# Performance work log

Measured on AMD Instinct MI355X. Metric: run time of the kernel, lower is better.

The kernel has to match this reference:

```python
import jax, jax.numpy as jnp
import numpy as np

EMBED = 1024
HEADS = 16
HDIM = EMBED // HEADS


def setup_inputs() -> dict:
    key = jax.random.key(0)
    ks = jax.random.split(key, 7)
    N, T = 16, 1024
    s = 1.0 / np.sqrt(EMBED)
    X = jax.random.normal(ks[0], (N, T, EMBED), dtype=jnp.float32)
    mask = jax.random.randint(ks[1], (N, 1, T, T), 0, 2, dtype=jnp.int32)
    Wq = jax.random.normal(ks[2], (EMBED, EMBED), dtype=jnp.float32) * s
    Wk = jax.random.normal(ks[3], (EMBED, EMBED), dtype=jnp.float32) * s
    Wv = jax.random.normal(ks[4], (EMBED, EMBED), dtype=jnp.float32) * s
    Wo = jax.random.normal(ks[5], (EMBED, EMBED), dtype=jnp.float32) * s
    bo = jax.random.normal(ks[6], (EMBED,), dtype=jnp.float32) * 0.01
    return {"X": X, "mask": mask, "Wq": Wq, "Wk": Wk, "Wv": Wv, "Wo": Wo, "bo": bo}


def reference(X, mask, Wq, Wk, Wv, Wo, bo):
    N, T, K = X.shape
    # QKV projections (Linear with bias=False): y = x @ W^T
    def proj(W):
        y = jnp.einsum('btk,ok->bto', X, W)          # [N, T, K]
        return y.reshape(N, T, HEADS, HDIM).transpose(0, 2, 1, 3)  # [N, H, T, hd]
    q, k, v = proj(Wq), proj(Wk), proj(Wv)
    # scaled dot-product scores; note source scales by sqrt(embed_size), not sqrt(head_dim)
    scores = jnp.einsum('bhqd,bhkd->bhqk', q, k) / jnp.sqrt(jnp.float32(K))
    scores = jnp.where(mask == 0, jnp.float32(-1e20), scores)
    attn = jax.nn.softmax(scores, axis=-1)
    out = jnp.einsum('bhqk,bhkd->bhqd', attn, v)     # [N, H, T, hd]
    out = out.transpose(0, 2, 1, 3).reshape(N, T, K)  # [N, T, K]
    return jnp.einsum('btk,ok->bto', out, Wo) + bo
```

## Files before the change

kernel.cpp:

```cpp
#include <hip/hip_runtime.h>
#include <hip/hip_bf16.h>

#define EMBED 1024
#define TSEQ  1024
#define NB    16
#define NH    16
#define HD    64
#define MROWS (NB * TSEQ)

typedef __bf16 bf16x8 __attribute__((ext_vector_type(8)));
typedef float  f32x4  __attribute__((ext_vector_type(4)));

__device__ __forceinline__ unsigned int f2bf_bits(float x) {
    union { float f; unsigned int u; } v; v.f = x;
    unsigned int r = v.u + 0x7FFFu + ((v.u >> 16) & 1u);
    return r >> 16;
}

__device__ __forceinline__ int detect_bf16(const unsigned int* __restrict__ X) {
    __shared__ int s_cnt;
    if (threadIdx.x == 0) s_cnt = 0;
    __syncthreads();
    int c = 0;
    const int base = threadIdx.x * 16;
#pragma unroll
    for (int i = 0; i < 16; ++i) {
        unsigned int e = (X[base + i] >> 7) & 0xFFu;
        c += (e >= 100u && e <= 150u) ? 1 : 0;
    }
    atomicAdd(&s_cnt, c);
    __syncthreads();
    return s_cnt >= 2458;
}

__device__ __forceinline__ uint4 load8(const void* __restrict__ p, size_t eoff,
                                       int is_bf16) {
    if (is_bf16) {
        return *(const uint4*)((const __hip_bfloat16*)p + eoff);
    }
    const float* f = (const float*)p + eoff;
    float4 a = *(const float4*)f;
    float4 b = *(const float4*)(f + 4);
    uint4 r;
    r.x = f2bf_bits(a.x) | (f2bf_bits(a.y) << 16);
    r.y = f2bf_bits(a.z) | (f2bf_bits(a.w) << 16);
    r.z = f2bf_bits(b.x) | (f2bf_bits(b.y) << 16);
    r.w = f2bf_bits(b.z) | (f2bf_bits(b.w) << 16);
    return r;
}

__device__ __forceinline__ void gload16(const __hip_bfloat16* g,
                                        __hip_bfloat16* l) {
    __builtin_amdgcn_global_load_lds(
        (const __attribute__((address_space(1))) void*)g,
        (__attribute__((address_space(3))) void*)l, 16, 0, 0);
}

__global__ __launch_bounds__(256) void to_bf16(
    const void* __restrict__ src, __hip_bfloat16* __restrict__ dst,
    int n8, const unsigned int* __restrict__ det)
{
    const int isbf = detect_bf16(det);
    const int i = blockIdx.x * 256 + threadIdx.x;
    if (i < n8) *(uint4*)(dst + (size_t)i * 8) = load8(src, (size_t)i * 8, isbf);
}

#define BK  32
#define LDK 40

template<int AD, int BD>
__global__ __launch_bounds__(256) void gemm_t(
    const void* __restrict__ A,
    const void* __restrict__ W,
    void* __restrict__ C,
    const void* __restrict__ bias,
    const unsigned int* __restrict__ Xdet,
    int a_flex, int out_mode, float cscale)
{
    const int isbf = detect_bf16(Xdet);
    const int a_bf = a_flex ? isbf : 1;

    constexpr int LA = AD ? BK : LDK;
    constexpr int LB = BD ? BK : LDK;
    __shared__ __hip_bfloat16 As[128 * LA];
    __shared__ __hip_bfloat16 Bs[128 * LB];

    const int tid  = threadIdx.x;
    const int lane = tid & 63;
    const int w    = tid >> 6;
    const int wm   = w & 1;
    const int wn   = w >> 1;
    const int m0   = blockIdx.x * 128;
    const int n0   = blockIdx.y * 128;

    const int r0 = tid >> 2;
    const int c0 = (tid & 3) * 8;

    f32x4 acc[4][4];
#pragma unroll
    for (int i = 0; i < 4; ++i)
#pragma unroll
        for (int j = 0; j < 4; ++j)
            acc[i][j] = (f32x4){0.f, 0.f, 0.f, 0.f};

    const int fr = lane & 15;
    const int fq = lane >> 4;

    for (int k0 = 0; k0 < EMBED; k0 += BK) {
        uint4 ra0, ra1, rb0, rb1;
        if constexpr (!AD) {
            ra0 = load8(A, (size_t)(m0 + r0)      * EMBED + c0 + k0, a_bf);
            ra1 = load8(A, (size_t)(m0 + r0 + 64) * EMBED + c0 + k0, a_bf);
        }
        if constexpr (!BD) {
            rb0 = load8(W, (size_t)(n0 + r0)      * EMBED + c0 + k0, isbf);
            rb1 = load8(W, (size_t)(n0 + r0 + 64) * EMBED + c0 + k0, isbf);
        }
        __syncthreads();
        if constexpr (AD) {
            const __hip_bfloat16* Ab =
                (const __hip_bfloat16*)A + (size_t)(m0 + r0) * EMBED + c0 + k0;
            gload16(Ab,                      &As[tid * 8]);
            gload16(Ab + (size_t)64 * EMBED, &As[64 * BK + tid * 8]);
        } else {
            *(uint4*)&As[r0 * LA + c0]        = ra0;
            *(uint4*)&As[(r0 + 64) * LA + c0] = ra1;
        }
        if constexpr (BD) {
            const __hip_bfloat16* Wp =
                (const __hip_bfloat16*)W + (size_t)(n0 + r0) * EMBED + c0 + k0;
            gload16(Wp,                      &Bs[tid * 8]);
            gload16(Wp + (size_t)64 * EMBED, &Bs[64 * BK + tid * 8]);
        } else {
            *(uint4*)&Bs[r0 * LB + c0]        = rb0;
            *(uint4*)&Bs[(r0 + 64) * LB + c0] = rb1;
        }
        __syncthreads();

        bf16x8 af[4], bfr[4];
#pragma unroll
        for (int i = 0; i < 4; ++i) {
            af[i]  = *(const bf16x8*)&As[(wm * 64 + i * 16 + fr) * LA + fq * 8];
            bfr[i] = *(const bf16x8*)&Bs[(wn * 64 + i * 16 + fr) * LB + fq * 8];
        }
#pragma unroll
        for (int i = 0; i < 4; ++i)
#pragma unroll
            for (int j = 0; j < 4; ++j)
                acc[i][j] = __builtin_amdgcn_mfma_f32_16x16x32_bf16(
                    af[i], bfr[j], acc[i][j], 0, 0, 0);
    }

    float bv[4] = {0.f, 0.f, 0.f, 0.f};
    if (bias != nullptr) {
#pragma unroll
        for (int j = 0; j < 4; ++j) {
            const int idx = n0 + wn * 64 + j * 16 + fr;
            bv[j] = isbf ? __bfloat162float(((const __hip_bfloat16*)bias)[idx])
                         : ((const float*)bias)[idx];
        }
    }

    if (out_mode == 2) {
#pragma unroll
        for (int i = 0; i < 4; ++i) {
            const int row = m0 + wm * 64 + i * 16 + fq * 4;
            const int bb = row >> 10, tt = row & 1023;
#pragma unroll
            for (int j = 0; j < 4; ++j) {
                const int col = n0 + wn * 64 + j * 16 + fr;
                const int hh = col >> 6, dd = col & 63;
                uint2 st;
                st.x = f2bf_bits(acc[i][j][0] * cscale) |
                       (f2bf_bits(acc[i][j][1] * cscale) << 16);
                st.y = f2bf_bits(acc[i][j][2] * cscale) |
                       (f2bf_bits(acc[i][j][3] * cscale) << 16);
                *(uint2*)&((__hip_bfloat16*)C)[
                    (((size_t)(bb * NH + hh) * HD + dd) * TSEQ) + tt] = st;
            }
        }
        return;
    }

    const int c_bf = (out_mode == 1) ? isbf : 1;
#pragma unroll
    for (int i = 0; i < 4; ++i) {
        const int row = m0 + wm * 64 + i * 16 + fq * 4;
#pragma unroll
        for (int j = 0; j < 4; ++j) {
            const int col = n0 + wn * 64 + j * 16 + fr;
#pragma unroll
            for (int r = 0; r < 4; ++r) {
                const size_t off = (size_t)(row + r) * EMBED + col;
                const float v = acc[i][j][r] * cscale + bv[j];
                if (c_bf) ((__hip_bfloat16*)C)[off] = __float2bfloat16(v);
                else      ((float*)C)[off] = v;
            }
        }
    }
}

#define QT  64
#define KTL 128
#define KP  72
#define VP  136
#define PP  136

__global__ __launch_bounds__(256) void attn_mfma(
    const __hip_bfloat16* __restrict__ Q,
    const __hip_bfloat16* __restrict__ K,
    const __hip_bfloat16* __restrict__ Vt,
    const int* __restrict__ mask,
    __hip_bfloat16* __restrict__ O)
{
    __shared__ __hip_bfloat16 Ks[KTL * KP];
    __shared__ __hip_bfloat16 Vs[HD * VP];
    __shared__ __hip_bfloat16 Ps[4][16 * PP];

    const int tid  = threadIdx.x;
    const int lane = tid & 63;
    const int w    = tid >> 6;
    const int fr   = lane & 15;
    const int fq   = lane >> 4;
    const int qb = blockIdx.x, h = blockIdx.y, b = blockIdx.z;
    const int q0 = qb * QT;

    const __hip_bfloat16* qptr =
        Q + (size_t)(b * TSEQ + q0 + w * 16 + fr) * EMBED + h * HD + fq * 8;
    const bf16x8 qa0 = *(const bf16x8*)qptr;
    const bf16x8 qa1 = *(const bf16x8*)(qptr + 32);

    float mS[4], lS[4];
    f32x4 oacc[4];
#pragma unroll
    for (int r = 0; r < 4; ++r) { mS[r] = -1e29f; lS[r] = 0.f; }
#pragma unroll
    for (int dt = 0; dt < 4; ++dt) oacc[dt] = (f32x4){0.f, 0.f, 0.f, 0.f};

    for (int kt = 0; kt < TSEQ / KTL; ++kt) {
        __syncthreads();
#pragma unroll
        for (int i = 0; i < 4; ++i) {
            const int cc  = tid + 256 * i;
            const int key = cc >> 3;
            const int dc  = (cc & 7) * 8;
            *(uint4*)&Ks[key * KP + dc] = *(const uint4*)(
                K + (size_t)(b * TSEQ + kt * KTL + key) * EMBED + h * HD + dc);
            const int d  = cc >> 4;
            const int kc = (cc & 15) * 8;
            *(uint4*)&Vs[d * VP + kc] = *(const uint4*)(
                Vt + ((size_t)(b * NH + h) * HD + d) * TSEQ + kt * KTL + kc);
        }
        __syncthreads();

        const int* mbase = mask + (size_t)(b * TSEQ + q0 + w * 16 + fq * 4) * TSEQ
                           + kt * KTL + fr;
        int mv[8][4];
#pragma unroll
        for (int t = 0; t < 8; ++t)
#pragma unroll
            for (int r = 0; r < 4; ++r)
                mv[t][r] = mbase[r * TSEQ + t * 16];

        f32x4 s[8];
#pragma unroll
        for (int t = 0; t < 8; ++t) {
            const bf16x8 kb0 = *(const bf16x8*)&Ks[(t * 16 + fr) * KP + fq * 8];
            const bf16x8 kb1 = *(const bf16x8*)&Ks[(t * 16 + fr) * KP + 32 + fq * 8];
            s[t] = __builtin_amdgcn_mfma_f32_16x16x32_bf16(
                qa0, kb0, (f32x4){0.f, 0.f, 0.f, 0.f}, 0, 0, 0);
            s[t] = __builtin_amdgcn_mfma_f32_16x16x32_bf16(qa1, kb1, s[t], 0, 0, 0);
        }

#pragma unroll
        for (int t = 0; t < 8; ++t)
#pragma unroll
            for (int r = 0; r < 4; ++r)
                if (mv[t][r] == 0) s[t][r] = -1e30f;

#pragma unroll
        for (int r = 0; r < 4; ++r) {
            float mx = s[0][r];
#pragma unroll
            for (int t = 1; t < 8; ++t) mx = fmaxf(mx, s[t][r]);
#pragma unroll
            for (int off = 8; off > 0; off >>= 1) mx = fmaxf(mx, __shfl_xor(mx, off));
            const float mnew  = fmaxf(mS[r], mx);
            const float alpha = __builtin_amdgcn_exp2f(mS[r] - mnew);
            mS[r] = mnew;
            float ls = 0.f;
#pragma unroll
            for (int t = 0; t < 8; ++t) {
                const float p = __builtin_amdgcn_exp2f(s[t][r] - mnew);
                s[t][r] = p;
                ls += p;
            }
#pragma unroll
            for (int off = 8; off > 0; off >>= 1) ls += __shfl_xor(ls, off);
            lS[r] = lS[r] * alpha + ls;
#pragma unroll
            for (int dt = 0; dt < 4; ++dt) oacc[dt][r] *= alpha;
        }

#pragma unroll
        for (int t = 0; t < 8; ++t)
#pragma unroll
            for (int r = 0; r < 4; ++r)
                Ps[w][(fq * 4 + r) * PP + t * 16 + fr] = __float2bfloat16(s[t][r]);

#pragma unroll
        for (int kc = 0; kc < 4; ++kc) {
            const bf16x8 pa = *(const bf16x8*)&Ps[w][fr * PP + kc * 32 + fq * 8];
#pragma unroll
            for (int dt = 0; dt < 4; ++dt) {
                const bf16x8 vb =
                    *(const bf16x8*)&Vs[(dt * 16 + fr) * VP + kc * 32 + fq * 8];
                oacc[dt] = __builtin_amdgcn_mfma_f32_16x16x32_bf16(
                    pa, vb, oacc[dt], 0, 0, 0);
            }
        }
    }

    float inv[4];
#pragma unroll
    for (int r = 0; r < 4; ++r) inv[r] = 1.f / fmaxf(lS[r], 1e-30f);
#pragma unroll
    for (int dt = 0; dt < 4; ++dt)
#pragma unroll
        for (int r = 0; r < 4; ++r)
            O[(size_t)(b * TSEQ + q0 + w * 16 + fq * 4 + r) * EMBED
              + h * HD + dt * 16 + fr] = __float2bfloat16(oacc[dt][r] * inv[r]);
}

static inline void launch_gemm(int ad, int bd, dim3 g, dim3 b, hipStream_t s,
                               const void* A, const void* W, void* C,
                               const void* bias, const unsigned int* Xdet,
                               int a_flex, int out_mode, float cs)
{
    if (ad && bd)
        gemm_t<1, 1><<<g, b, 0, s>>>(A, W, C, bias, Xdet, a_flex, out_mode, cs);
    else if (ad)
        gemm_t<1, 0><<<g, b, 0, s>>>(A, W, C, bias, Xdet, a_flex, out_mode, cs);
    else if (bd)
        gemm_t<0, 1><<<g, b, 0, s>>>(A, W, C, bias, Xdet, a_flex, out_mode, cs);
    else
        gemm_t<0, 0><<<g, b, 0, s>>>(A, W, C, bias, Xdet, a_flex, out_mode, cs);
}

extern "C" void kernel_launch(void* const* d_in, const int* in_sizes, int n_in,
                              void* d_out, int out_size, void* d_ws, size_t ws_size,
                              hipStream_t stream) {
    const void* X  = d_in[0];
    const int*  Mk = (const int*)d_in[1];
    const void* Wsrc[4] = { d_in[2], d_in[3], d_in[4], d_in[5] };
    const void* bo = d_in[6];
    const unsigned int* Xdet = (const unsigned int*)d_in[0];

    const size_t n_elem = (size_t)MROWS * EMBED;
    const size_t w_elem = (size_t)EMBED * EMBED;
    __hip_bfloat16* Qb  = (__hip_bfloat16*)d_ws;
    __hip_bfloat16* Kb  = Qb + n_elem;
    __hip_bfloat16* Vtb = (__hip_bfloat16*)d_out;
    size_t ws_used = 2 * n_elem * sizeof(__hip_bfloat16);

    dim3 blk(256);

    const void* Ax = X;
    int ad = 0;
    if (in_sizes[0] == (int)(n_elem * 2)) {
        ad = 1;
    } else {
        __hip_bfloat16* Xb = nullptr;
        if ((size_t)out_size >= n_elem * 4) {
            Xb = (__hip_bfloat16*)d_out + n_elem;
        } else if (ws_size >= ws_used + n_elem * 2) {
            Xb = (__hip_bfloat16*)((char*)d_ws + ws_used);
            ws_used += n_elem * 2;
        }
        if (Xb) {
            to_bf16<<<dim3((unsigned)(n_elem / 8 / 256)), blk, 0, stream>>>(
                X, Xb, (int)(n_elem / 8), Xdet);
            Ax = Xb;
            ad = 1;
        }
    }

    const void* Wb[4];
    int bd = 0;
    if (in_sizes[2] == (int)(w_elem * 2)) {
        for (int i = 0; i < 4; ++i) Wb[i] = Wsrc[i];
        bd = 1;
    } else if (ws_size >= ws_used + 4 * w_elem * 2) {
        __hip_bfloat16* p = (__hip_bfloat16*)((char*)d_ws + ws_used);
        for (int i = 0; i < 4; ++i) {
            to_bf16<<<dim3((unsigned)(w_elem / 8 / 256)), blk, 0, stream>>>(
                Wsrc[i], p + (size_t)i * w_elem, (int)(w_elem / 8), Xdet);
            Wb[i] = p + (size_t)i * w_elem;
        }
        ws_used += 4 * w_elem * 2;
        bd = 1;
    } else {
        for (int i = 0; i < 4; ++i) Wb[i] = Wsrc[i];
    }

    dim3 gg(MROWS / 128, EMBED / 128, 1);
    const float qs = 0.03125f * 1.44269504088896f;
    launch_gemm(ad, bd, gg, blk, stream, Ax, Wb[0], Qb,  nullptr, Xdet, 1, 0, qs);
    launch_gemm(ad, bd, gg, blk, stream, Ax, Wb[1], Kb,  nullptr, Xdet, 1, 0, 1.f);
    launch_gemm(ad, bd, gg, blk, stream, Ax, Wb[2], Vtb, nullptr, Xdet, 1, 2, 1.f);

    dim3 ga(TSEQ / QT, NH, NB);
    attn_mfma<<<ga, blk, 0, stream>>>(Qb, Kb, Vtb, Mk, Qb);

    launch_gemm(1, bd, gg, blk, stream, Qb, Wb[3], d_out, bo, Xdet, 0, 1, 1.f);
}
```

Before: 666.2 us.

## Bit-pack attention mask once and prefetch next K/V tile into registers

Adds a pre-pass that packs the int32 mask into one bit per element with wave ballots. The attention kernel then reads the packed words instead of re-reading the full int32 mask once per head. The K/V tile loads are also register-prefetched one iteration ahead, so global loads overlap compute and one barrier is replaced with a manual waitcnt plus s_barrier. The cost is an extra kernel and scratch space, which is taken from the output or workspace buffer, and the kernel falls back to the int32 mask when no space is available.

```diff
diff --git a/kernel.cpp b/kernel.cpp
--- a/kernel.cpp
+++ b/kernel.cpp
@@ -63,6 +63,16 @@
     const int isbf = detect_bf16(det);
     const int i = blockIdx.x * 256 + threadIdx.x;
     if (i < n8) *(uint4*)(dst + (size_t)i * 8) = load8(src, (size_t)i * 8, isbf);
+}
+
+__global__ __launch_bounds__(256) void pack_mask(
+    const int* __restrict__ m, unsigned* __restrict__ bm, int n)
+{
+    const int i = blockIdx.x * 256 + threadIdx.x;
+    const unsigned long long bal = __ballot(i < n && m[i] != 0);
+    if ((threadIdx.x & 31) == 0 && i < n) {
+        bm[i >> 5] = (unsigned)(((threadIdx.x & 63) < 32) ? bal : (bal >> 32));
+    }
 }
 
 #define BK  32
@@ -202,6 +212,7 @@
 
 #define QT  64
 #define KTL 128
+#define NT  (TSEQ / KTL)
 #define KP  72
 #define VP  136
 #define PP  136
@@ -211,6 +222,7 @@
     const __hip_bfloat16* __restrict__ K,
     const __hip_bfloat16* __restrict__ Vt,
     const int* __restrict__ mask,
+    const unsigned* __restrict__ bmask,
     __hip_bfloat16* __restrict__ O)
 {
     __shared__ __hip_bfloat16 Ks[KTL * KP];
@@ -230,6 +242,37 @@
     const bf16x8 qa0 = *(const bf16x8*)qptr;
     const bf16x8 qa1 = *(const bf16x8*)(qptr + 32);
 
+    const __hip_bfloat16* kg[4];
+    const __hip_bfloat16* vg[4];
+    int lk[4], lv[4];
+#pragma unroll
+    for (int i = 0; i < 4; ++i) {
+        const int cc  = tid + 256 * i;
+        const int key = cc >> 3;
+        const int dc  = (cc & 7) * 8;
+        kg[i] = K + (size_t)(b * TSEQ + key) * EMBED + h * HD + dc;
+        lk[i] = key * KP + dc;
+        const int d  = cc >> 4;
+        const int kc = (cc & 15) * 8;
+        vg[i] = Vt + ((size_t)(b * NH + h) * HD + d) * TSEQ + kc;
+        lv[i] = d * VP + kc;
+    }
+
+    uint4 kr[4], vr[4];
+#pragma unroll
+    for (int i = 0; i < 4; ++i) {
+        kr[i] = *(const uint4*)kg[i];
+        vr[i] = *(const uint4*)vg[i];
+    }
+
+    const unsigned* bmr[4];
+    if (bmask) {
+#pragma unroll
+        for (int r = 0; r < 4; ++r)
+            bmr[r] = bmask +
+                (size_t)(b * TSEQ + q0 + w * 16 + fq * 4 + r) * (TSEQ / 32);
+    }
+
     float mS[4], lS[4];
     f32x4 oacc[4];
 #pragma unroll
@@ -237,30 +280,39 @@
 #pragma unroll
     for (int dt = 0; dt < 4; ++dt) oacc[dt] = (f32x4){0.f, 0.f, 0.f, 0.f};
 
-    for (int kt = 0; kt < TSEQ / KTL; ++kt) {
+    for (int kt = 0; kt < NT; ++kt) {
         __syncthreads();
 #pragma unroll
         for (int i = 0; i < 4; ++i) {
-            const int cc  = tid + 256 * i;
-            const int key = cc >> 3;
-            const int dc  = (cc & 7) * 8;
-            *(uint4*)&Ks[key * KP + dc] = *(const uint4*)(
-                K + (size_t)(b * TSEQ + kt * KTL + key) * EMBED + h * HD + dc);
-            const int d  = cc >> 4;
-            const int kc = (cc & 15) * 8;
-            *(uint4*)&Vs[d * VP + kc] = *(const uint4*)(
-                Vt + ((size_t)(b * NH + h) * HD + d) * TSEQ + kt * KTL + kc);
-        }
-        __syncthreads();
-
-        const int* mbase = mask + (size_t)(b * TSEQ + q0 + w * 16 + fq * 4) * TSEQ
-                           + kt * KTL + fr;
-        int mv[8][4];
-#pragma unroll
-        for (int t = 0; t < 8; ++t)
+            *(uint4*)&Ks[lk[i]] = kr[i];
+            *(uint4*)&Vs[lv[i]] = vr[i];
+        }
+        if (kt + 1 < NT) {
+#pragma unroll
+            for (int i = 0; i < 4; ++i) {
+                kr[i] = *(const uint4*)(kg[i] + (size_t)(kt + 1) * KTL * EMBED);
+                vr[i] = *(const uint4*)(vg[i] + (kt + 1) * KTL);
+            }
+        }
+        asm volatile("s_waitcnt lgkmcnt(0)" ::: "memory");
+        __builtin_amdgcn_s_barrier();
+        __builtin_amdgcn_sched_barrier(0);
+
+        uint4 mw[4];
+        int mvf[8][4];
+        if (bmask) {
 #pragma unroll
             for (int r = 0; r < 4; ++r)
-                mv[t][r] = mbase[r * TSEQ + t * 16];
+                mw[r] = *(const uint4*)(bmr[r] + kt * 4);
+        } else {
+            const int* mbase = mask +
+                (size_t)(b * TSEQ + q0 + w * 16 + fq * 4) * TSEQ + kt * KTL + fr;
+#pragma unroll
+            for (int t = 0; t < 8; ++t)
+#pragma unroll
+                for (int r = 0; r < 4; ++r)
+                    mvf[t][r] = mbase[r * TSEQ + t * 16];
+        }
 
         f32x4 s[8];
 #pragma unroll
@@ -272,11 +324,21 @@
             s[t] = __builtin_amdgcn_mfma_f32_16x16x32_bf16(qa1, kb1, s[t], 0, 0, 0);
         }
 
-#pragma unroll
-        for (int t = 0; t < 8; ++t)
-#pragma unroll
-            for (int r = 0; r < 4; ++r)
-                if (mv[t][r] == 0) s[t][r] = -1e30f;
+        if (bmask) {
+#pragma unroll
+            for (int t = 0; t < 8; ++t)
+#pragma unroll
+                for (int r = 0; r < 4; ++r) {
+                    const unsigned wv = ((const unsigned*)&mw[r])[t >> 1] >> fr;
+                    if (((wv >> ((t & 1) * 16)) & 1u) == 0u) s[t][r] = -1e30f;
+                }
+        } else {
+#pragma unroll
+            for (int t = 0; t < 8; ++t)
+#pragma unroll
+                for (int r = 0; r < 4; ++r)
+                    if (mvf[t][r] == 0) s[t][r] = -1e30f;
+        }
 
 #pragma unroll
         for (int r = 0; r < 4; ++r) {
@@ -403,14 +465,29 @@
         for (int i = 0; i < 4; ++i) Wb[i] = Wsrc[i];
     }
 
+    const size_t bm_words = (size_t)NB * TSEQ * (TSEQ / 32);
+    const size_t bm_bytes = bm_words * 4;
+    unsigned* bm = nullptr;
+    if ((size_t)out_size >= n_elem * 2 + bm_bytes) {
+        bm = (unsigned*)((char*)d_out + n_elem * 2);
+    } else if (ws_size >= ws_used + bm_bytes) {
+        bm = (unsigned*)((char*)d_ws + ws_used);
+        ws_used += bm_bytes;
+    }
+
     dim3 gg(MROWS / 128, EMBED / 128, 1);
     const float qs = 0.03125f * 1.44269504088896f;
     launch_gemm(ad, bd, gg, blk, stream, Ax, Wb[0], Qb,  nullptr, Xdet, 1, 0, qs);
     launch_gemm(ad, bd, gg, blk, stream, Ax, Wb[1], Kb,  nullptr, Xdet, 1, 0, 1.f);
     launch_gemm(ad, bd, gg, blk, stream, Ax, Wb[2], Vtb, nullptr, Xdet, 1, 2, 1.f);
 
+    if (bm) {
+        const int nmask = NB * TSEQ * TSEQ;
+        pack_mask<<<dim3(nmask / 256), blk, 0, stream>>>(Mk, bm, nmask);
+    }
+
     dim3 ga(TSEQ / QT, NH, NB);
-    attn_mfma<<<ga, blk, 0, stream>>>(Qb, Kb, Vtb, Mk, Qb);
+    attn_mfma<<<ga, blk, 0, stream>>>(Qb, Kb, Vtb, Mk, bm, Qb);
 
     launch_gemm(1, bd, gg, blk, stream, Qb, Wb[3], d_out, bo, Xdet, 0, 1, 1.f);
 }
```

New measurement: 820.2 us. +23.1%, slower.
